# Kernel tuning notes

Measured on AMD Instinct MI355X. Metric: run time of the kernel, lower is better.

The kernel has to match this reference:

```python
import jax, jax.numpy as jnp
import numpy as np

NUM_SCALE_LAYERS = [16, 8, 8]


def _pool2s1(x):
    # MaxPool1d(kernel=2, stride=1): length L -> L-1
    return jnp.maximum(x[..., :-1], x[..., 1:])


def _pool3s2(x):
    # MaxPool1d(kernel=3, stride=2): length L -> (L-3)//2 + 1
    L = x.shape[-1]
    n = (L - 3) // 2 + 1
    return jnp.maximum(jnp.maximum(x[..., 0:2 * n:2], x[..., 1:2 * n + 1:2]),
                       x[..., 2:2 * n + 2:2])


def setup_inputs() -> dict:
    key = jax.random.key(0)
    x = jax.random.normal(key, (32, 512, 64), dtype=jnp.float32)
    return {"x": x}


def reference(x):
    B, H, N = x.shape
    ori = N  # scale 0 has stride-1 first layer, so ori_num_clips == N
    map_h = jnp.zeros((B, H, ori, ori), dtype=x.dtype)
    map_mask = jnp.zeros((B, 1, ori, ori), dtype=x.dtype)
    acum = 0
    stride = 1
    for scale_idx, num_layer in enumerate(NUM_SCALE_LAYERS):
        for i in range(num_layer):
            if i == 0:
                if scale_idx > 0:
                    x = _pool3s2(x)
                    stride *= 2
                # scale 0 first layer is MaxPool1d(1,1) == identity, stride*=1
            else:
                x = _pool2s1(x)
            # diagonal scatter directly into the original-resolution map
            s_idx = np.arange(0, ori - acum - i * stride, stride)
            e_idx = s_idx + acum + i * stride
            map_h = map_h.at[:, :, s_idx, e_idx].set(x)
            map_mask = map_mask.at[:, :, s_idx, e_idx].set(jnp.ones((), x.dtype))
        acum += stride * (num_layer + 1)
    return map_h, map_mask
```

## Files before the change

kernel.cpp:

```cpp
#include <hip/hip_runtime.h>


#define BB 32
#define HH 512
#define NN 64

typedef float f32x4 __attribute__((ext_vector_type(4)));

__device__ __forceinline__ unsigned long long active_mask_for_e(int e) {
    unsigned long long m;
    if (e >= 15) m = 0xFFFFull << (e - 15);
    else         m = 0xFFFFull >> (15 - e);
    if ((e & 1) && e >= 17) {
        int a = e - 31; if (a < 0) a = 0;
        int b = e - 17;
        unsigned long long r = (~0ull >> (63 - b)) & (~0ull << a);
        m |= r & 0x5555555555555555ull;
    }
    if (((e & 3) == 3) && e >= 35) {
        int b = e - 35;
        unsigned long long r = (~0ull >> (63 - b));
        m |= r & 0x1111111111111111ull;
    }
    return m;
}

__global__ __launch_bounds__(256) void sppool_fused_kernel(
        const float* __restrict__ x, float* __restrict__ map_h,
        float* __restrict__ map_mask) {
    __shared__ float xs[16][65];
    const int tid  = threadIdx.x;
    const int lrow = tid >> 4;
    const int e0   = (tid & 15) << 2;
    const size_t rowbase = (size_t)blockIdx.x * 16;

    const float* xin = x + rowbase * NN;
    #pragma unroll
    for (int i = 0; i < 4; ++i) {
        const int j = i * 256 + tid;
        xs[j >> 6][j & 63] = xin[j];
    }
    __syncthreads();

    const float* xr = xs[lrow];
    const unsigned long long am0 = active_mask_for_e(e0 + 0);
    const unsigned long long am1 = active_mask_for_e(e0 + 1);
    const unsigned long long am2 = active_mask_for_e(e0 + 2);
    const unsigned long long am3 = active_mask_for_e(e0 + 3);

    float m0 = -INFINITY, m1 = -INFINITY, m2 = -INFINITY, m3 = -INFINITY;
    float* out = map_h + (rowbase + lrow) * (NN * NN) + e0;

    #pragma unroll 8
    for (int s = 63; s >= 0; --s) {
        const float xv = xr[s];
        m0 = fmaxf(m0, (s <= e0 + 0) ? xv : -INFINITY);
        m1 = fmaxf(m1, (s <= e0 + 1) ? xv : -INFINITY);
        m2 = fmaxf(m2, (s <= e0 + 2) ? xv : -INFINITY);
        m3 = fmaxf(m3, (s <= e0 + 3) ? xv : -INFINITY);
        f32x4 v;
        v.x = ((am0 >> s) & 1ull) ? m0 : 0.0f;
        v.y = ((am1 >> s) & 1ull) ? m1 : 0.0f;
        v.z = ((am2 >> s) & 1ull) ? m2 : 0.0f;
        v.w = ((am3 >> s) & 1ull) ? m3 : 0.0f;
        __builtin_nontemporal_store(
            v, reinterpret_cast<f32x4*>(out + (size_t)s * NN));
    }

    if (blockIdx.x < BB) {
        f32x4* mout = reinterpret_cast<f32x4*>(
            map_mask + (size_t)blockIdx.x * (NN * NN));
        #pragma unroll
        for (int k = 0; k < 4; ++k) {
            const int idx = k * 256 + tid;
            const int eg  = (idx & 15) << 2;
            const int s   = idx >> 4;
            f32x4 v;
            v.x = ((active_mask_for_e(eg + 0) >> s) & 1ull) ? 1.0f : 0.0f;
            v.y = ((active_mask_for_e(eg + 1) >> s) & 1ull) ? 1.0f : 0.0f;
            v.z = ((active_mask_for_e(eg + 2) >> s) & 1ull) ? 1.0f : 0.0f;
            v.w = ((active_mask_for_e(eg + 3) >> s) & 1ull) ? 1.0f : 0.0f;
            __builtin_nontemporal_store(v, mout + idx);
        }
    }
}

extern "C" void kernel_launch(void* const* d_in, const int* in_sizes, int n_in,
                              void* d_out, int out_size, void* d_ws, size_t ws_size,
                              hipStream_t stream) {
    const float* x = (const float*)d_in[0];
    float* map_h    = (float*)d_out;
    float* map_mask = (float*)d_out + (size_t)BB * HH * NN * NN;

    sppool_fused_kernel<<<BB * HH / 16, 256, 0, stream>>>(x, map_h, map_mask);
}
```

Baseline: 264.0 us.

## Use sparse-table range max and rotate per-row store order

Builds a sparse table of power-of-two window maxima in shared memory, so each output's range max comes from two lookups instead of a serial running max over s. The store loop also starts at a per-row phase offset, which spreads concurrent writes from different rows across memory channels. The kernel is mostly bound by the 268MB output write, so the extra shared-memory passes and barriers may add cost without saving much.

```diff
diff --git a/kernel.cpp b/kernel.cpp
--- a/kernel.cpp
+++ b/kernel.cpp
@@ -28,41 +28,62 @@
 __global__ __launch_bounds__(256) void sppool_fused_kernel(
         const float* __restrict__ x, float* __restrict__ map_h,
         float* __restrict__ map_mask) {
-    __shared__ float xs[16][65];
+    __shared__ float sp[16][7][68];
+
     const int tid  = threadIdx.x;
     const int lrow = tid >> 4;
-    const int e0   = (tid & 15) << 2;
+    const int lcol = tid & 15;
+    const int e0   = lcol << 2;
     const size_t rowbase = (size_t)blockIdx.x * 16;
 
     const float* xin = x + rowbase * NN;
-    #pragma unroll
-    for (int i = 0; i < 4; ++i) {
-        const int j = i * 256 + tid;
-        xs[j >> 6][j & 63] = xin[j];
-    }
+    const f32x4 xv = ((const f32x4*)xin)[tid];
+    *(f32x4*)&sp[lrow][0][e0] = xv;
     __syncthreads();
 
-    const float* xr = xs[lrow];
+    #pragma unroll
+    for (int k = 1; k <= 6; ++k) {
+        const int off = 1 << (k - 1);
+        float v[4];
+        #pragma unroll
+        for (int ii = 0; ii < 4; ++ii) {
+            const int i = lcol + ii * 16;
+            int p = i + off; if (p > 63) p = 63;
+            v[ii] = fmaxf(sp[lrow][k - 1][i], sp[lrow][k - 1][p]);
+        }
+        __syncthreads();
+        #pragma unroll
+        for (int ii = 0; ii < 4; ++ii)
+            sp[lrow][k][lcol + ii * 16] = v[ii];
+        __syncthreads();
+    }
+
     const unsigned long long am0 = active_mask_for_e(e0 + 0);
     const unsigned long long am1 = active_mask_for_e(e0 + 1);
     const unsigned long long am2 = active_mask_for_e(e0 + 2);
     const unsigned long long am3 = active_mask_for_e(e0 + 3);
 
-    float m0 = -INFINITY, m1 = -INFINITY, m2 = -INFINITY, m3 = -INFINITY;
-    float* out = map_h + (rowbase + lrow) * (NN * NN) + e0;
+    const int grow  = (int)rowbase + lrow;
+    const int phase = (grow * 37) & 63;
+    const float* rowsp = &sp[lrow][0][0];
+    float* out = map_h + (size_t)grow * (NN * NN) + e0;
 
     #pragma unroll 8
-    for (int s = 63; s >= 0; --s) {
-        const float xv = xr[s];
-        m0 = fmaxf(m0, (s <= e0 + 0) ? xv : -INFINITY);
-        m1 = fmaxf(m1, (s <= e0 + 1) ? xv : -INFINITY);
-        m2 = fmaxf(m2, (s <= e0 + 2) ? xv : -INFINITY);
-        m3 = fmaxf(m3, (s <= e0 + 3) ? xv : -INFINITY);
+    for (int it = 0; it < 64; ++it) {
+        const int s = (63 - it + phase) & 63;
         f32x4 v;
-        v.x = ((am0 >> s) & 1ull) ? m0 : 0.0f;
-        v.y = ((am1 >> s) & 1ull) ? m1 : 0.0f;
-        v.z = ((am2 >> s) & 1ull) ? m2 : 0.0f;
-        v.w = ((am3 >> s) & 1ull) ? m3 : 0.0f;
+        #pragma unroll
+        for (int j = 0; j < 4; ++j) {
+            const int e = e0 + j;
+            int n = e - s + 1; if (n < 1) n = 1;
+            const int k = 31 - __clz(n);
+            const float lo = rowsp[k * 68 + s];
+            const float hi = rowsp[k * 68 + (e + 1 - (1 << k))];
+            const unsigned long long am = (j == 0) ? am0 : (j == 1) ? am1
+                                        : (j == 2) ? am2 : am3;
+            const float mv = fmaxf(lo, hi);
+            v[j] = ((am >> s) & 1ull) ? mv : 0.0f;
+        }
         __builtin_nontemporal_store(
             v, reinterpret_cast<f32x4*>(out + (size_t)s * NN));
     }
@@ -71,8 +92,8 @@
         f32x4* mout = reinterpret_cast<f32x4*>(
             map_mask + (size_t)blockIdx.x * (NN * NN));
         #pragma unroll
-        for (int k = 0; k < 4; ++k) {
-            const int idx = k * 256 + tid;
+        for (int kk = 0; kk < 4; ++kk) {
+            const int idx = kk * 256 + tid;
             const int eg  = (idx & 15) << 2;
             const int s   = idx >> 4;
             f32x4 v;
```

New measurement: 336.1 us. 27.3% more time.
